# Kernel tuning notes

Hardware: AMD Instinct MI355X
Metric: run time of the kernel (lower is better)

## Reference

```python
import jax, jax.numpy as jnp
import numpy as np

B, S, D, H = 2, 4096, 512, 8
HD = D // H

def setup_inputs() -> dict:
    key = jax.random.key(0)
    ks = jax.random.split(key, 11)
    s = 1.0 / np.sqrt(D)
    return {
        "x": jax.random.normal(ks[0], (B, S, D), jnp.float32),
        "y": jax.random.normal(ks[1], (B, S, D), jnp.float32),
        "z": jax.random.normal(ks[2], (B, S, D), jnp.float32),
        "Wq": jax.random.normal(ks[3], (D, D), jnp.float32) * s,
        "bq": jnp.zeros((D,), jnp.float32),
        "Wk": jax.random.normal(ks[4], (D, D), jnp.float32) * s,
        "bk": jnp.zeros((D,), jnp.float32),
        "Wv": jax.random.normal(ks[5], (D, D), jnp.float32) * s,
        "bv": jnp.zeros((D,), jnp.float32),
        "Wp": jax.random.normal(ks[6], (D, D), jnp.float32) * s,
        "bp": jnp.zeros((D,), jnp.float32),
    }

def reference(x, y, z, Wq, bq, Wk, bk, Wv, bv, Wp, bp):
    # q/k/v projections, split heads: [B,S,D] -> [B,H,S,HD]
    def heads(t):
        return t.reshape(B, -1, H, HD).transpose(0, 2, 1, 3)
    q = heads(x @ Wq + bq)
    k = heads(y @ Wk + bk)
    v = heads(z @ Wv + bv)
    att = jnp.einsum('bhqd,bhkd->bhqk', q, k) / np.sqrt(HD).astype(np.float32)
    att = jax.nn.softmax(att, axis=-1)  # dropout is identity in eval mode
    out = jnp.einsum('bhqk,bhkd->bhqd', att, v)
    out = out.transpose(0, 2, 1, 3).reshape(B, -1, D)
    return out @ Wp + bp
```

## Files before the change

kernel.cpp:

```cpp
#include <hip/hip_runtime.h>
#include <math.h>

#define B_ 2
#define S_ 4096
#define D_ 512
#define H_ 8
#define HD_ 64
#define NROW_ (B_ * S_)
#define NELEM_ ((size_t)NROW_ * D_)
#define WELEM_ ((size_t)D_ * D_)

typedef _Float16 half8 __attribute__((ext_vector_type(8)));
typedef _Float16 half4v __attribute__((ext_vector_type(4)));
typedef _Float16 half2v __attribute__((ext_vector_type(2)));
typedef __fp16 fp16x2 __attribute__((ext_vector_type(2)));
typedef float floatx4 __attribute__((ext_vector_type(4)));

__device__ __forceinline__ half8 cvt_half8(float4 a, float4 b) {
  fp16x2 l0 = __builtin_amdgcn_cvt_pkrtz(a.x, a.y);
  fp16x2 l1 = __builtin_amdgcn_cvt_pkrtz(a.z, a.w);
  fp16x2 l2 = __builtin_amdgcn_cvt_pkrtz(b.x, b.y);
  fp16x2 l3 = __builtin_amdgcn_cvt_pkrtz(b.z, b.w);
  half8 h;
  h[0] = l0[0]; h[1] = l0[1]; h[2] = l1[0]; h[3] = l1[1];
  h[4] = l2[0]; h[5] = l2[1]; h[6] = l3[0]; h[7] = l3[1];
  return h;
}

struct WPtrs { const float *W0, *W1, *W2, *W3; };

__global__ void wT4_kernel(WPtrs p, _Float16* __restrict__ WTbase) {
  __shared__ float tl[32][33];
  const int z = blockIdx.z;
  const float* W = z == 0 ? p.W0 : z == 1 ? p.W1 : z == 2 ? p.W2 : p.W3;
  const float scale = z == 0 ? 0.125f : 1.0f;
  _Float16* Wt = WTbase + (size_t)z * WELEM_;
  const int t = threadIdx.x;
  const int k0 = blockIdx.y * 32, n0 = blockIdx.x * 32;
  const int r = t >> 3, c0 = (t & 7) * 4;
  const float4 v = *(const float4*)&W[(size_t)(k0 + r) * D_ + n0 + c0];
  tl[r][c0 + 0] = v.x; tl[r][c0 + 1] = v.y;
  tl[r][c0 + 2] = v.z; tl[r][c0 + 3] = v.w;
  __syncthreads();
  half4v hv;
#pragma unroll
  for (int j = 0; j < 4; ++j) hv[j] = (_Float16)(tl[c0 + j][r] * scale);
  *(half4v*)&Wt[(size_t)(n0 + r) * D_ + k0 + c0] = hv;
}

__global__ void vT_kernel(const _Float16* __restrict__ Vh,
                          _Float16* __restrict__ VhT) {
  __shared__ alignas(16) _Float16 T[64][72];
  const int t = threadIdx.x;
  const int s0 = blockIdx.x * 64;
  const int h = blockIdx.y, b = blockIdx.z;
  const int srow = t >> 3, soff = (t & 7) * 8;
#pragma unroll
  for (int i = 0; i < 2; ++i)
    *(half8*)&T[srow + 32 * i][soff] = *(const half8*)
        &Vh[(size_t)(b * S_ + s0 + srow + 32 * i) * D_ + h * HD_ + soff];
  __syncthreads();
  const size_t obase = (size_t)(b * H_ + h) * HD_ * S_;
#pragma unroll
  for (int i = 0; i < 2; ++i) {
    half8 o;
#pragma unroll
    for (int j = 0; j < 8; ++j) {
      const int ka = soff + j;
      const int key = 16 * (ka & 3) + (ka >> 2);
      o[j] = T[key][srow + 32 * i];
    }
    *(half8*)&VhT[obase + (size_t)(srow + 32 * i) * S_ + s0 + soff] = o;
  }
}

template <bool AF16, bool OUT16, int BM>
__device__ __forceinline__ void gemm_body(
    const void* __restrict__ Av, const _Float16* __restrict__ Bt,
    const float* __restrict__ bias, void* __restrict__ Cout, float bscale,
    int bx, int by, int tid) {
  constexpr int MT = BM / 32;
  __shared__ alignas(16) _Float16 As[BM][72];
  __shared__ alignas(16) _Float16 Bs[128][72];

  const int w = tid >> 6, lane = tid & 63;
  const int m = lane & 15, quad = lane >> 4;
  const int row0 = by * BM, col0 = bx * 128;
  const int wr = (w >> 1) * (BM / 2), wc = (w & 1) * 64;
  const int srow = tid >> 3, soff = (tid & 7) * 8;

  const _Float16* A16 = (const _Float16*)Av;
  const float* A32 = (const float*)Av;

  floatx4 acc[MT][4];
#pragma unroll
  for (int i = 0; i < MT; ++i)
#pragma unroll
    for (int j = 0; j < 4; ++j) acc[i][j] = floatx4{0.f, 0.f, 0.f, 0.f};

  half8 pa16[MT];
  float4 pa32[MT][2];
  half8 pb[4];
#pragma unroll
  for (int i = 0; i < MT; ++i) {
    const size_t ar = (size_t)(row0 + srow + 32 * i) * D_ + soff;
    if (AF16) pa16[i] = *(const half8*)&A16[ar];
    else { pa32[i][0] = *(const float4*)&A32[ar];
           pa32[i][1] = *(const float4*)&A32[ar + 4]; }
  }
#pragma unroll
  for (int i = 0; i < 4; ++i)
    pb[i] = *(const half8*)&Bt[(size_t)(col0 + srow + 32 * i) * D_ + soff];

  for (int kt = 0; kt < D_ / 64; ++kt) {
    if (kt) __syncthreads();
#pragma unroll
    for (int i = 0; i < MT; ++i)
      *(half8*)&As[srow + 32 * i][soff] =
          AF16 ? pa16[i] : cvt_half8(pa32[i][0], pa32[i][1]);
#pragma unroll
    for (int i = 0; i < 4; ++i) *(half8*)&Bs[srow + 32 * i][soff] = pb[i];
    __syncthreads();
    if (kt < D_ / 64 - 1) {
      const int kc = (kt + 1) * 64 + soff;
#pragma unroll
      for (int i = 0; i < MT; ++i) {
        const size_t ar = (size_t)(row0 + srow + 32 * i) * D_ + kc;
        if (AF16) pa16[i] = *(const half8*)&A16[ar];
        else { pa32[i][0] = *(const float4*)&A32[ar];
               pa32[i][1] = *(const float4*)&A32[ar + 4]; }
      }
#pragma unroll
      for (int i = 0; i < 4; ++i)
        pb[i] = *(const half8*)&Bt[(size_t)(col0 + srow + 32 * i) * D_ + kc];
    }
#pragma unroll
    for (int h = 0; h < 2; ++h) {
      half8 af[MT], bf[4];
#pragma unroll
      for (int mt = 0; mt < MT; ++mt)
        af[mt] = *(const half8*)&As[wr + mt * 16 + m][h * 32 + quad * 8];
#pragma unroll
      for (int nt = 0; nt < 4; ++nt)
        bf[nt] = *(const half8*)&Bs[wc + nt * 16 + m][h * 32 + quad * 8];
#pragma unroll
      for (int mt = 0; mt < MT; ++mt)
#pragma unroll
        for (int nt = 0; nt < 4; ++nt)
          acc[mt][nt] = __builtin_amdgcn_mfma_f32_16x16x32_f16(
              af[mt], bf[nt], acc[mt][nt], 0, 0, 0);
    }
  }

  float bv[4];
#pragma unroll
  for (int nt = 0; nt < 4; ++nt)
    bv[nt] = bias[col0 + wc + nt * 16 + m] * bscale;
#pragma unroll
  for (int mt = 0; mt < MT; ++mt)
#pragma unroll
    for (int nt = 0; nt < 4; ++nt)
#pragma unroll
      for (int r = 0; r < 4; ++r) {
        const int row = row0 + wr + mt * 16 + quad * 4 + r;
        const int col = col0 + wc + nt * 16 + m;
        const float vout = acc[mt][nt][r] + bv[nt];
        if (OUT16)
          ((_Float16*)Cout)[(size_t)row * D_ + col] = (_Float16)vout;
        else
          ((float*)Cout)[(size_t)row * D_ + col] = vout;
      }
}

struct QkvPtrs { const float *A0, *A1, *A2, *b0, *b1, *b2; };

__global__ __launch_bounds__(256, 3) void qkv_gemm_kernel(
    QkvPtrs p, const _Float16* __restrict__ WT, _Float16* __restrict__ Cb) {
  const int z = blockIdx.z;
  const float* A = z == 0 ? p.A0 : z == 1 ? p.A1 : p.A2;
  const float* bias = z == 0 ? p.b0 : z == 1 ? p.b1 : p.b2;
  gemm_body<false, true, 128>(A, WT + (size_t)z * WELEM_, bias,
                              Cb + (size_t)z * NELEM_, z == 0 ? 0.125f : 1.0f,
                              blockIdx.x, blockIdx.y, threadIdx.x);
}

__global__ __launch_bounds__(256, 2) void out_gemm_kernel(
    const _Float16* __restrict__ Oh, const _Float16* __restrict__ WpT,
    const float* __restrict__ bp, float* __restrict__ out) {
  gemm_body<true, false, 64>(Oh, WpT, bp, out, 1.0f, blockIdx.x, blockIdx.y,
                             threadIdx.x);
}

__global__ __launch_bounds__(256, 2) void attn_mfma_kernel(
    const _Float16* __restrict__ Qg, const _Float16* __restrict__ Kg,
    const _Float16* __restrict__ VT, _Float16* __restrict__ Og) {
  __shared__ alignas(16) _Float16 Ks[64][72];
  __shared__ alignas(16) _Float16 Vt[64][72];
  __shared__ alignas(16) _Float16 Ps[128][72];

  const int t = threadIdx.x;
  const int w = t >> 6;
  const int lane = t & 63;
  const int m = lane & 15;
  const int quad = lane >> 4;
  const int q0 = blockIdx.x * 128;
  const size_t base =
      (size_t)blockIdx.z * ((size_t)S_ * D_) + (size_t)blockIdx.y * HD_;
  const size_t vbase = (size_t)(blockIdx.z * H_ + blockIdx.y) * HD_ * S_;

  half8 qf[2][2];
#pragma unroll
  for (int s = 0; s < 2; ++s)
#pragma unroll
    for (int h = 0; h < 2; ++h)
      qf[s][h] = *(const half8*)&Qg[base +
          (size_t)(q0 + s * 64 + w * 16 + m) * D_ + h * 32 + quad * 8];

  floatx4 oacc[2][4];
  float lpart[2][4];
#pragma unroll
  for (int s = 0; s < 2; ++s)
#pragma unroll
    for (int n = 0; n < 4; ++n) oacc[s][n] = floatx4{0.f, 0.f, 0.f, 0.f};
#pragma unroll
  for (int s = 0; s < 2; ++s)
#pragma unroll
    for (int r = 0; r < 4; ++r) lpart[s][r] = 0.f;

  const int srow = t >> 3, soff = (t & 7) * 8;

  half8 pk[2], pv[2];
#pragma unroll
  for (int i = 0; i < 2; ++i) {
    pk[i] = *(const half8*)&Kg[base + (size_t)(srow + 32 * i) * D_ + soff];
    pv[i] = *(const half8*)&VT[vbase + (size_t)(srow + 32 * i) * S_ + soff];
  }

  for (int kt = 0; kt < S_ / 64; ++kt) {
    if (kt) __syncthreads();
#pragma unroll
    for (int i = 0; i < 2; ++i) {
      *(half8*)&Ks[srow + 32 * i][soff] = pk[i];
      *(half8*)&Vt[srow + 32 * i][soff] = pv[i];
    }
    __syncthreads();

    if (kt < S_ / 64 - 1) {
      const int k1 = (kt + 1) * 64;
#pragma unroll
      for (int i = 0; i < 2; ++i) {
        pk[i] = *(const half8*)
            &Kg[base + (size_t)(k1 + srow + 32 * i) * D_ + soff];
        pv[i] = *(const half8*)
            &VT[vbase + (size_t)(srow + 32 * i) * S_ + k1 + soff];
      }
    }

    floatx4 sacc[2][4];
#pragma unroll
    for (int s = 0; s < 2; ++s)
#pragma unroll
      for (int n = 0; n < 4; ++n) sacc[s][n] = floatx4{0.f, 0.f, 0.f, 0.f};
#pragma unroll
    for (int n = 0; n < 4; ++n)
#pragma unroll
      for (int h = 0; h < 2; ++h) {
        const half8 bf = *(const half8*)&Ks[n * 16 + m][h * 32 + quad * 8];
        sacc[0][n] = __builtin_amdgcn_mfma_f32_16x16x32_f16(
            qf[0][h], bf, sacc[0][n], 0, 0, 0);
        sacc[1][n] = __builtin_amdgcn_mfma_f32_16x16x32_f16(
            qf[1][h], bf, sacc[1][n], 0, 0, 0);
      }

#pragma unroll
    for (int s = 0; s < 2; ++s) {
      const int prow = s * 64 + w * 16 + quad * 4;
#pragma unroll
      for (int r = 0; r < 4; ++r) {
        const float p0 = __expf(fminf(sacc[s][0][r], 11.f));
        const float p1 = __expf(fminf(sacc[s][1][r], 11.f));
        const float p2 = __expf(fminf(sacc[s][2][r], 11.f));
        const float p3 = __expf(fminf(sacc[s][3][r], 11.f));
        lpart[s][r] += (p0 + p1) + (p2 + p3);
        const fp16x2 plo = __builtin_amdgcn_cvt_pkrtz(p0, p1);
        const fp16x2 phi = __builtin_amdgcn_cvt_pkrtz(p2, p3);
        half4v ph;
        ph[0] = plo[0]; ph[1] = plo[1]; ph[2] = phi[0]; ph[3] = phi[1];
        *(half4v*)&Ps[prow + r][4 * m] = ph;
      }
    }

    half8 af[2][2];
#pragma unroll
    for (int s = 0; s < 2; ++s) {
      af[s][0] = *(const half8*)&Ps[s * 64 + w * 16 + m][quad * 8];
      af[s][1] = *(const half8*)&Ps[s * 64 + w * 16 + m][32 + quad * 8];
    }
#pragma unroll
    for (int n = 0; n < 4; ++n) {
      const half8 b0 = *(const half8*)&Vt[n * 16 + m][quad * 8];
      const half8 b1 = *(const half8*)&Vt[n * 16 + m][32 + quad * 8];
#pragma unroll
      for (int s = 0; s < 2; ++s) {
        oacc[s][n] = __builtin_amdgcn_mfma_f32_16x16x32_f16(
            af[s][0], b0, oacc[s][n], 0, 0, 0);
        oacc[s][n] = __builtin_amdgcn_mfma_f32_16x16x32_f16(
            af[s][1], b1, oacc[s][n], 0, 0, 0);
      }
    }
  }

  float linv[2][4];
#pragma unroll
  for (int s = 0; s < 2; ++s)
#pragma unroll
    for (int r = 0; r < 4; ++r) {
      float ls = lpart[s][r];
      ls += __shfl_xor(ls, 1);
      ls += __shfl_xor(ls, 2);
      ls += __shfl_xor(ls, 4);
      ls += __shfl_xor(ls, 8);
      linv[s][r] = 1.0f / ls;
    }
#pragma unroll
  for (int s = 0; s < 2; ++s)
#pragma unroll
    for (int n = 0; n < 4; ++n)
#pragma unroll
      for (int r = 0; r < 4; ++r)
        Og[base + (size_t)(q0 + s * 64 + w * 16 + quad * 4 + r) * D_ +
           n * 16 + m] = (_Float16)(oacc[s][n][r] * linv[s][r]);
}

extern "C" void kernel_launch(void* const* d_in, const int* in_sizes, int n_in,
                              void* d_out, int out_size, void* d_ws,
                              size_t ws_size, hipStream_t stream) {
  const float* x  = (const float*)d_in[0];
  const float* y  = (const float*)d_in[1];
  const float* z  = (const float*)d_in[2];
  const float* Wq = (const float*)d_in[3];
  const float* bq = (const float*)d_in[4];
  const float* Wk = (const float*)d_in[5];
  const float* bk = (const float*)d_in[6];
  const float* Wv = (const float*)d_in[7];
  const float* bv = (const float*)d_in[8];
  const float* Wp = (const float*)d_in[9];
  const float* bp = (const float*)d_in[10];

  _Float16* hws = (_Float16*)d_ws;
  _Float16* WT  = hws;
  _Float16* Qh  = WT + 4 * WELEM_;
  _Float16* Kh  = Qh + NELEM_;
  _Float16* Vh  = Kh + NELEM_;
  _Float16* Oh  = Vh + NELEM_;
  _Float16* VhT = Oh + NELEM_;

  WPtrs wp{Wq, Wk, Wv, Wp};
  wT4_kernel<<<dim3(16, 16, 4), 256, 0, stream>>>(wp, WT);

  QkvPtrs qp{x, y, z, bq, bk, bv};
  qkv_gemm_kernel<<<dim3(4, 64, 3), 256, 0, stream>>>(qp, WT, Qh);

  vT_kernel<<<dim3(S_ / 64, H_, B_), 256, 0, stream>>>(Vh, VhT);

  attn_mfma_kernel<<<dim3(S_ / 128, H_, B_), 256, 0, stream>>>(Qh, Kh, VhT, Oh);

  out_gemm_kernel<<<dim3(4, 128), 256, 0, stream>>>(Oh, WT + 3 * WELEM_, bp,
                                                    (float*)d_out);
}
```

Baseline: 260.7 us.

## Split keys across waves in attention, drop shared-memory staging of K/V/P

The attention kernel now gives each of the four waves its own slice of every 64-key tile. K and V^T fragments are loaded straight from global memory into registers, and P is computed in transposed form so it can feed the PV MFMA without a round trip through shared memory. The per-iteration __syncthreads and LDS staging go away, replaced by a serialized cross-wave reduction of output and row sums in LDS at the end. Query tiles shrink to 64 per block, which doubles the grid and raises the occupancy hint. The V transpose kernel's key permutation is also removed to match the new fragment layout. The trade-off is uncoalesced direct global fragment loads with no prefetch, plus more K/V traffic per query.

```diff
diff --git a/kernel.cpp b/kernel.cpp
--- a/kernel.cpp
+++ b/kernel.cpp
@@ -12,7 +12,6 @@
 
 typedef _Float16 half8 __attribute__((ext_vector_type(8)));
 typedef _Float16 half4v __attribute__((ext_vector_type(4)));
-typedef _Float16 half2v __attribute__((ext_vector_type(2)));
 typedef __fp16 fp16x2 __attribute__((ext_vector_type(2)));
 typedef float floatx4 __attribute__((ext_vector_type(4)));
 
@@ -65,11 +64,7 @@
   for (int i = 0; i < 2; ++i) {
     half8 o;
 #pragma unroll
-    for (int j = 0; j < 8; ++j) {
-      const int ka = soff + j;
-      const int key = 16 * (ka & 3) + (ka >> 2);
-      o[j] = T[key][srow + 32 * i];
-    }
+    for (int j = 0; j < 8; ++j) o[j] = T[soff + j][srow + 32 * i];
     *(half8*)&VhT[obase + (size_t)(srow + 32 * i) * S_ + s0 + soff] = o;
   }
 }
@@ -191,145 +186,128 @@
                              threadIdx.x);
 }
 
-__global__ __launch_bounds__(256, 2) void attn_mfma_kernel(
+__global__ __launch_bounds__(256, 3) void attn_v2_kernel(
     const _Float16* __restrict__ Qg, const _Float16* __restrict__ Kg,
     const _Float16* __restrict__ VT, _Float16* __restrict__ Og) {
-  __shared__ alignas(16) _Float16 Ks[64][72];
-  __shared__ alignas(16) _Float16 Vt[64][72];
-  __shared__ alignas(16) _Float16 Ps[128][72];
+  __shared__ float ored[64][67];
+  __shared__ float lred[4][64];
 
   const int t = threadIdx.x;
-  const int w = t >> 6;
-  const int lane = t & 63;
-  const int m = lane & 15;
-  const int quad = lane >> 4;
-  const int q0 = blockIdx.x * 128;
+  const int w = t >> 6, lane = t & 63;
+  const int m = lane & 15, quad = lane >> 4;
+  const int q0 = blockIdx.x * 64;
   const size_t base =
       (size_t)blockIdx.z * ((size_t)S_ * D_) + (size_t)blockIdx.y * HD_;
   const size_t vbase = (size_t)(blockIdx.z * H_ + blockIdx.y) * HD_ * S_;
 
-  half8 qf[2][2];
-#pragma unroll
-  for (int s = 0; s < 2; ++s)
-#pragma unroll
-    for (int h = 0; h < 2; ++h)
-      qf[s][h] = *(const half8*)&Qg[base +
-          (size_t)(q0 + s * 64 + w * 16 + m) * D_ + h * 32 + quad * 8];
-
-  floatx4 oacc[2][4];
-  float lpart[2][4];
-#pragma unroll
-  for (int s = 0; s < 2; ++s)
-#pragma unroll
-    for (int n = 0; n < 4; ++n) oacc[s][n] = floatx4{0.f, 0.f, 0.f, 0.f};
-#pragma unroll
-  for (int s = 0; s < 2; ++s)
-#pragma unroll
-    for (int r = 0; r < 4; ++r) lpart[s][r] = 0.f;
-
-  const int srow = t >> 3, soff = (t & 7) * 8;
-
-  half8 pk[2], pv[2];
-#pragma unroll
-  for (int i = 0; i < 2; ++i) {
-    pk[i] = *(const half8*)&Kg[base + (size_t)(srow + 32 * i) * D_ + soff];
-    pv[i] = *(const half8*)&VT[vbase + (size_t)(srow + 32 * i) * S_ + soff];
-  }
+  half8 qb[4][2];
+#pragma unroll
+  for (int nt = 0; nt < 4; ++nt)
+#pragma unroll
+    for (int hh = 0; hh < 2; ++hh)
+      qb[nt][hh] = *(const half8*)
+          &Qg[base + (size_t)(q0 + 16 * nt + m) * D_ + 32 * hh + 8 * quad];
+
+  floatx4 oacc[4][4];
+  float lpart[4];
+#pragma unroll
+  for (int i = 0; i < 4; ++i) {
+    lpart[i] = 0.f;
+#pragma unroll
+    for (int j = 0; j < 4; ++j) oacc[i][j] = floatx4{0.f, 0.f, 0.f, 0.f};
+  }
+
+  const _Float16* kp = Kg + base + (size_t)(16 * w + m) * D_ + 8 * quad;
+  const _Float16* vp0 = VT + vbase + (size_t)m * S_ + 16 * w + 4 * quad;
+  const _Float16* vp1 = vp0 + (size_t)16 * S_;
+  const _Float16* vp2 = vp0 + (size_t)32 * S_;
+  const _Float16* vp3 = vp0 + (size_t)48 * S_;
 
   for (int kt = 0; kt < S_ / 64; ++kt) {
-    if (kt) __syncthreads();
-#pragma unroll
-    for (int i = 0; i < 2; ++i) {
-      *(half8*)&Ks[srow + 32 * i][soff] = pk[i];
-      *(half8*)&Vt[srow + 32 * i][soff] = pv[i];
+    half8 ka0 = *(const half8*)kp;
+    half8 ka1 = *(const half8*)(kp + 32);
+    half4v va[4];
+    va[0] = *(const half4v*)vp0;
+    va[1] = *(const half4v*)vp1;
+    va[2] = *(const half4v*)vp2;
+    va[3] = *(const half4v*)vp3;
+    kp += (size_t)64 * D_;
+    vp0 += 64; vp1 += 64; vp2 += 64; vp3 += 64;
+
+    floatx4 sacc[4];
+#pragma unroll
+    for (int nt = 0; nt < 4; ++nt) {
+      floatx4 s = floatx4{0.f, 0.f, 0.f, 0.f};
+      s = __builtin_amdgcn_mfma_f32_16x16x32_f16(ka0, qb[nt][0], s, 0, 0, 0);
+      s = __builtin_amdgcn_mfma_f32_16x16x32_f16(ka1, qb[nt][1], s, 0, 0, 0);
+      sacc[nt] = s;
+    }
+
+    half4v pbf[4];
+#pragma unroll
+    for (int nt = 0; nt < 4; ++nt) {
+      const float p0 = __expf(fminf(sacc[nt][0], 11.f));
+      const float p1 = __expf(fminf(sacc[nt][1], 11.f));
+      const float p2 = __expf(fminf(sacc[nt][2], 11.f));
+      const float p3 = __expf(fminf(sacc[nt][3], 11.f));
+      lpart[nt] += (p0 + p1) + (p2 + p3);
+      const fp16x2 lo = __builtin_amdgcn_cvt_pkrtz(p0, p1);
+      const fp16x2 hi = __builtin_amdgcn_cvt_pkrtz(p2, p3);
+      half4v pb;
+      pb[0] = lo[0]; pb[1] = lo[1]; pb[2] = hi[0]; pb[3] = hi[1];
+      pbf[nt] = pb;
+    }
+
+#pragma unroll
+    for (int mt = 0; mt < 4; ++mt)
+#pragma unroll
+      for (int nt = 0; nt < 4; ++nt)
+        oacc[mt][nt] = __builtin_amdgcn_mfma_f32_16x16x16f16(
+            va[mt], pbf[nt], oacc[mt][nt], 0, 0, 0);
+  }
+
+#pragma unroll
+  for (int nt = 0; nt < 4; ++nt) {
+    float v = lpart[nt];
+    v += __shfl_xor(v, 16);
+    v += __shfl_xor(v, 32);
+    lpart[nt] = v;
+  }
+  if (quad == 0) {
+#pragma unroll
+    for (int nt = 0; nt < 4; ++nt) lred[w][16 * nt + m] = lpart[nt];
+  }
+
+  for (int wv = 0; wv < 4; ++wv) {
+    if (w == wv) {
+#pragma unroll
+      for (int mt = 0; mt < 4; ++mt)
+#pragma unroll
+        for (int nt = 0; nt < 4; ++nt)
+#pragma unroll
+          for (int r = 0; r < 4; ++r) {
+            const int d = 16 * mt + 4 * quad + r;
+            const int qq = 16 * nt + m;
+            float v = oacc[mt][nt][r];
+            if (wv) v += ored[d][qq];
+            ored[d][qq] = v;
+          }
     }
     __syncthreads();
-
-    if (kt < S_ / 64 - 1) {
-      const int k1 = (kt + 1) * 64;
-#pragma unroll
-      for (int i = 0; i < 2; ++i) {
-        pk[i] = *(const half8*)
-            &Kg[base + (size_t)(k1 + srow + 32 * i) * D_ + soff];
-        pv[i] = *(const half8*)
-            &VT[vbase + (size_t)(srow + 32 * i) * S_ + k1 + soff];
-      }
-    }
-
-    floatx4 sacc[2][4];
-#pragma unroll
-    for (int s = 0; s < 2; ++s)
-#pragma unroll
-      for (int n = 0; n < 4; ++n) sacc[s][n] = floatx4{0.f, 0.f, 0.f, 0.f};
-#pragma unroll
-    for (int n = 0; n < 4; ++n)
-#pragma unroll
-      for (int h = 0; h < 2; ++h) {
-        const half8 bf = *(const half8*)&Ks[n * 16 + m][h * 32 + quad * 8];
-        sacc[0][n] = __builtin_amdgcn_mfma_f32_16x16x32_f16(
-            qf[0][h], bf, sacc[0][n], 0, 0, 0);
-        sacc[1][n] = __builtin_amdgcn_mfma_f32_16x16x32_f16(
-            qf[1][h], bf, sacc[1][n], 0, 0, 0);
-      }
-
-#pragma unroll
-    for (int s = 0; s < 2; ++s) {
-      const int prow = s * 64 + w * 16 + quad * 4;
-#pragma unroll
-      for (int r = 0; r < 4; ++r) {
-        const float p0 = __expf(fminf(sacc[s][0][r], 11.f));
-        const float p1 = __expf(fminf(sacc[s][1][r], 11.f));
-        const float p2 = __expf(fminf(sacc[s][2][r], 11.f));
-        const float p3 = __expf(fminf(sacc[s][3][r], 11.f));
-        lpart[s][r] += (p0 + p1) + (p2 + p3);
-        const fp16x2 plo = __builtin_amdgcn_cvt_pkrtz(p0, p1);
-        const fp16x2 phi = __builtin_amdgcn_cvt_pkrtz(p2, p3);
-        half4v ph;
-        ph[0] = plo[0]; ph[1] = plo[1]; ph[2] = phi[0]; ph[3] = phi[1];
-        *(half4v*)&Ps[prow + r][4 * m] = ph;
-      }
-    }
-
-    half8 af[2][2];
-#pragma unroll
-    for (int s = 0; s < 2; ++s) {
-      af[s][0] = *(const half8*)&Ps[s * 64 + w * 16 + m][quad * 8];
-      af[s][1] = *(const half8*)&Ps[s * 64 + w * 16 + m][32 + quad * 8];
-    }
-#pragma unroll
-    for (int n = 0; n < 4; ++n) {
-      const half8 b0 = *(const half8*)&Vt[n * 16 + m][quad * 8];
-      const half8 b1 = *(const half8*)&Vt[n * 16 + m][32 + quad * 8];
-#pragma unroll
-      for (int s = 0; s < 2; ++s) {
-        oacc[s][n] = __builtin_amdgcn_mfma_f32_16x16x32_f16(
-            af[s][0], b0, oacc[s][n], 0, 0, 0);
-        oacc[s][n] = __builtin_amdgcn_mfma_f32_16x16x32_f16(
-            af[s][1], b1, oacc[s][n], 0, 0, 0);
-      }
-    }
-  }
-
-  float linv[2][4];
-#pragma unroll
-  for (int s = 0; s < 2; ++s)
-#pragma unroll
-    for (int r = 0; r < 4; ++r) {
-      float ls = lpart[s][r];
-      ls += __shfl_xor(ls, 1);
-      ls += __shfl_xor(ls, 2);
-      ls += __shfl_xor(ls, 4);
-      ls += __shfl_xor(ls, 8);
-      linv[s][r] = 1.0f / ls;
-    }
-#pragma unroll
-  for (int s = 0; s < 2; ++s)
-#pragma unroll
-    for (int n = 0; n < 4; ++n)
-#pragma unroll
-      for (int r = 0; r < 4; ++r)
-        Og[base + (size_t)(q0 + s * 64 + w * 16 + quad * 4 + r) * D_ +
-           n * 16 + m] = (_Float16)(oacc[s][n][r] * linv[s][r]);
+  }
+
+  const int qq = t >> 2, dg = (t & 3) * 16;
+  const float li =
+      1.0f / (lred[0][qq] + lred[1][qq] + lred[2][qq] + lred[3][qq]);
+  half8 o0, o1;
+#pragma unroll
+  for (int j = 0; j < 8; ++j) {
+    o0[j] = (_Float16)(ored[dg + j][qq] * li);
+    o1[j] = (_Float16)(ored[dg + 8 + j][qq] * li);
+  }
+  _Float16* op = Og + base + (size_t)(q0 + qq) * D_ + dg;
+  *(half8*)op = o0;
+  *(half8*)(op + 8) = o1;
 }
 
 extern "C" void kernel_launch(void* const* d_in, const int* in_sizes, int n_in,
@@ -363,7 +341,7 @@
 
   vT_kernel<<<dim3(S_ / 64, H_, B_), 256, 0, stream>>>(Vh, VhT);
 
-  attn_mfma_kernel<<<dim3(S_ / 128, H_, B_), 256, 0, stream>>>(Qh, Kh, VhT, Oh);
+  attn_v2_kernel<<<dim3(S_ / 64, H_, B_), 256, 0, stream>>>(Qh, Kh, VhT, Oh);
 
   out_gemm_kernel<<<dim3(4, 128), 256, 0, stream>>>(Oh, WT + 3 * WELEM_, bp,
                                                     (float*)d_out);
```

New measurement: 336.0 us. 28.9% more time.
